# Kernel optimization log

Measured on AMD Instinct MI355X. Metric: run time of the kernel, lower is better.

## Reference

```python
import jax, jax.numpy as jnp
import numpy as np

N = 50000   # nodes
E = 800000  # edges (before self-loops)
IN, H1, H2, OUT = 128, 256, 256, 64


def _gcn_layer(x, src, dst, norm_src, norm_dst, W, b, act):
    # DGL GraphConv, norm='both': D_in^{-1/2} * A^T * (D_out^{-1/2} * x) @ W + b
    x = x * norm_src                                   # [N, d_in]
    m = jax.ops.segment_sum(x[src], dst, num_segments=N)  # gather + scatter-add
    h = (m * norm_dst) @ W + b                         # [N, d_out]
    return act(h) if act is not None else h


def setup_inputs() -> dict:
    key = jax.random.key(0)
    ks = jax.random.split(key, 9)
    feats = jax.random.normal(ks[0], (N, IN), dtype=jnp.float32)
    src = jax.random.randint(ks[1], (E,), 0, N, dtype=jnp.int32)
    dst = jax.random.randint(ks[2], (E,), 0, N, dtype=jnp.int32)
    # avoid pre-existing self-loops (forward removes then re-adds exactly one per node)
    dst = jnp.where(src == dst, (dst + 1) % N, dst)
    def glorot(k, fi, fo):
        lim = float(np.sqrt(6.0 / (fi + fo)))
        return jax.random.uniform(k, (fi, fo), jnp.float32, -lim, lim)
    return {
        "feats": feats,
        "W1": glorot(ks[3], IN, H1), "b1": jnp.zeros((H1,), jnp.float32),
        "W2": glorot(ks[4], H1, H2), "b2": jnp.zeros((H2,), jnp.float32),
        "W3": glorot(ks[5], H2, OUT), "b3": jnp.zeros((OUT,), jnp.float32),
        "src": src, "dst": dst,
    }


def reference(feats, W1, b1, W2, b2, W3, b3, src, dst):
    # add self-loops
    loops = jnp.arange(N, dtype=src.dtype)
    s = jnp.concatenate([src, loops])
    d = jnp.concatenate([dst, loops])
    ones = jnp.ones(s.shape[0], jnp.float32)
    out_deg = jax.ops.segment_sum(ones, s, num_segments=N)
    in_deg = jax.ops.segment_sum(ones, d, num_segments=N)
    norm_src = (out_deg ** -0.5)[:, None]
    norm_dst = (in_deg ** -0.5)[:, None]
    relu = jax.nn.relu
    h = _gcn_layer(feats, s, d, norm_src, norm_dst, W1, b1, relu)
    # dropout p=0.0 (eval) is identity
    h = _gcn_layer(h, s, d, norm_src, norm_dst, W2, b2, relu)
    h = _gcn_layer(h, s, d, norm_src, norm_dst, W3, b3, None)
    return h
```

## Files before the change

### kernel.cpp

```cpp
#include <hip/hip_runtime.h>
#include <hip/hip_fp16.h>
#include <stdint.h>

#define NODES 50000
#define F_IN 128
#define F_H1 256
#define F_H2 256
#define F_OUT 64
#define SLICES 64
#define NPACK (NODES / 2)
#define HPACK (NPACK / 2)

using f32x4    = __attribute__((ext_vector_type(4))) float;
using f16x8    = __attribute__((ext_vector_type(8))) _Float16;
using ushort8v = __attribute__((ext_vector_type(8))) unsigned short;

__global__ __launch_bounds__(512) void k_hist(
    const int* __restrict__ src, const int* __restrict__ dst,
    unsigned* __restrict__ p_out, unsigned* __restrict__ p_in, int e) {
  __shared__ unsigned bins[HPACK];
  const int s = blockIdx.x >> 1;
  const int r = blockIdx.x & 1;
  const int nlo = r * (NODES / 2);
  const int nhi = nlo + NODES / 2;
  const int plo = r * HPACK;
  const int per = (e + SLICES - 1) / SLICES;
  const int beg = s * per;
  const int end = min(e, beg + per);

  for (int j = threadIdx.x; j < HPACK; j += 512) bins[j] = 0;
  __syncthreads();
  for (int i = beg + (int)threadIdx.x; i < end; i += 512) {
    int a = src[i];
    if (a >= nlo && a < nhi)
      atomicAdd(&bins[(a >> 1) - plo], 1u << ((a & 1) << 4));
  }
  __syncthreads();
  for (int j = threadIdx.x; j < HPACK; j += 512)
    p_out[(size_t)s * NPACK + plo + j] = bins[j];
  __syncthreads();

  for (int j = threadIdx.x; j < HPACK; j += 512) bins[j] = 0;
  __syncthreads();
  for (int i = beg + (int)threadIdx.x; i < end; i += 512) {
    int d = dst[i];
    if (d >= nlo && d < nhi)
      atomicAdd(&bins[(d >> 1) - plo], 1u << ((d & 1) << 4));
  }
  __syncthreads();
  for (int j = threadIdx.x; j < HPACK; j += 512)
    p_in[(size_t)s * NPACK + plo + j] = bins[j];
}

__global__ __launch_bounds__(256) void k_degnorm(
    const unsigned* __restrict__ p_out, const unsigned* __restrict__ p_in,
    unsigned* __restrict__ base_in, int* __restrict__ deg_in,
    float* __restrict__ ns, float* __restrict__ nd) {
  int p = blockIdx.x * 256 + threadIdx.x;
  if (p >= NPACK) return;
  unsigned so = 0, si = 0;
#pragma unroll 4
  for (int s = 0; s < SLICES; ++s) {
    so += p_out[(size_t)s * NPACK + p];
    unsigned vi = p_in[(size_t)s * NPACK + p];
    base_in[(size_t)s * NPACK + p] = si;
    si += vi;
  }
  int o0 = (int)(so & 0xFFFFu) + 1, o1 = (int)(so >> 16) + 1;
  int i0 = (int)(si & 0xFFFFu) + 1, i1 = (int)(si >> 16) + 1;
  int n0 = p * 2, n1 = n0 + 1;
  deg_in[n0] = i0; deg_in[n1] = i1;
  ns[n0] = rsqrtf((float)o0); ns[n1] = rsqrtf((float)o1);
  nd[n0] = rsqrtf((float)i0); nd[n1] = rsqrtf((float)i1);
}

__global__ __launch_bounds__(256) void k_scan1(const int* __restrict__ deg_in,
                                               int* __restrict__ psum, int n) {
  int i = blockIdx.x * 256 + threadIdx.x;
  int v = (i < n) ? deg_in[i] - 1 : 0;
#pragma unroll
  for (int o = 1; o < 64; o <<= 1) v += __shfl_xor(v, o);
  __shared__ int ws[4];
  if ((threadIdx.x & 63) == 0) ws[threadIdx.x >> 6] = v;
  __syncthreads();
  if (threadIdx.x == 0) psum[blockIdx.x] = ws[0] + ws[1] + ws[2] + ws[3];
}

__global__ __launch_bounds__(256) void k_scan2(int* __restrict__ psum, int nb) {
  __shared__ int s[256];
  int t = threadIdx.x;
  int v = (t < nb) ? psum[t] : 0;
  s[t] = v;
  __syncthreads();
  for (int o = 1; o < 256; o <<= 1) {
    int u = (t >= o) ? s[t - o] : 0;
    __syncthreads();
    s[t] += u;
    __syncthreads();
  }
  if (t < nb) psum[t] = s[t] - v;
}

__global__ __launch_bounds__(256) void k_scan3(const int* __restrict__ deg_in,
                                               const int* __restrict__ psum,
                                               int* __restrict__ row_ptr, int n) {
  int i = blockIdx.x * 256 + threadIdx.x;
  int lane = threadIdx.x & 63;
  int w = threadIdx.x >> 6;
  int v = (i < n) ? deg_in[i] - 1 : 0;
  int x = v;
#pragma unroll
  for (int o = 1; o < 64; o <<= 1) {
    int u = __shfl_up(x, o);
    if (lane >= o) x += u;
  }
  __shared__ int wsum[4];
  if (lane == 63) wsum[w] = x;
  __syncthreads();
  int woff = 0;
#pragma unroll
  for (int j = 0; j < 4; ++j)
    if (j < w) woff += wsum[j];
  int excl = x - v + woff + psum[blockIdx.x];
  if (i < n) row_ptr[i] = excl;
  if (i == n - 1) row_ptr[n] = excl + v;
}

__global__ __launch_bounds__(512) void k_scatter2(
    const int* __restrict__ src, const int* __restrict__ dst,
    const int* __restrict__ row_ptr, const unsigned* __restrict__ base_in,
    int* __restrict__ csr_src, int e) {
  __shared__ unsigned cur[HPACK];
  const int s = blockIdx.x >> 1;
  const int r = blockIdx.x & 1;
  const int nlo = r * (NODES / 2);
  const int nhi = nlo + NODES / 2;
  const int plo = r * HPACK;
  const int per = (e + SLICES - 1) / SLICES;
  const int beg = s * per;
  const int end = min(e, beg + per);
  for (int j = threadIdx.x; j < HPACK; j += 512)
    cur[j] = base_in[(size_t)s * NPACK + plo + j];
  __syncthreads();
  for (int i = beg + (int)threadIdx.x; i < end; i += 512) {
    int d = dst[i];
    if (d >= nlo && d < nhi) {
      int sh = (d & 1) << 4;
      unsigned old = atomicAdd(&cur[(d >> 1) - plo], 1u << sh);
      int local = (int)((old >> sh) & 0xFFFFu);
      csr_src[row_ptr[d] + local] = src[i];
    }
  }
}

__global__ void k_prescale_h(const float* __restrict__ X, const float* __restrict__ ns,
                             __half* __restrict__ Y, int total4) {
  int i = blockIdx.x * blockDim.x + threadIdx.x;
  if (i < total4) {
    int row = i >> 5;
    float s = ns[row];
    float4 v = reinterpret_cast<const float4*>(X)[i];
    __half2 h0 = __floats2half2_rn(v.x * s, v.y * s);
    __half2 h1 = __floats2half2_rn(v.z * s, v.w * s);
    union { struct { __half2 a, b; } h; uint2 u; } o;
    o.h.a = h0; o.h.b = h1;
    reinterpret_cast<uint2*>(Y)[i] = o.u;
  }
}

__global__ void k_wprep_h(const float* __restrict__ W, __half* __restrict__ Wt,
                          int K, int NOUT) {
  int i = blockIdx.x * blockDim.x + threadIdx.x;
  if (i < K * NOUT) {
    int k = i / NOUT, n = i % NOUT;
    Wt[(size_t)n * K + k] = __float2half_rn(W[i]);
  }
}

template <int HPL> struct raw_t_sel;
template <> struct raw_t_sel<2> { using type = unsigned int; };
template <> struct raw_t_sel<4> { using type = uint2; };
template <> struct raw_t_sel<8> { using type = uint4; };

template <int HPL>
__device__ __forceinline__ typename raw_t_sel<HPL>::type graw(const __half* p) {
  return *reinterpret_cast<const typename raw_t_sel<HPL>::type*>(p);
}
__device__ __forceinline__ void acc_u32(float* acc, unsigned u) {
  union { unsigned u; __half2 h; } a; a.u = u;
  float2 f = __half22float2(a.h);
  acc[0] += f.x; acc[1] += f.y;
}
template <int HPL>
__device__ __forceinline__ void raw_acc(float* acc, typename raw_t_sel<HPL>::type r) {
  if constexpr (HPL == 8) {
    acc_u32(acc + 0, r.x); acc_u32(acc + 2, r.y);
    acc_u32(acc + 4, r.z); acc_u32(acc + 6, r.w);
  } else if constexpr (HPL == 4) {
    acc_u32(acc + 0, r.x); acc_u32(acc + 2, r.y);
  } else {
    acc_u32(acc, r);
  }
}

template <int D, int EPI, bool BIAS, bool OHALF>
__global__ __launch_bounds__(256) void k_spmm_h(
    const __half* __restrict__ X, const int* __restrict__ row_ptr,
    const int* __restrict__ csr_src, const float* __restrict__ nd,
    const float* __restrict__ bias, void* __restrict__ Y, int n) {
  constexpr int LPN = 64 / EPI;
  constexpr int HPL = D / LPN;
  static_assert(HPL >= 2 && HPL <= 8, "bad HPL");
  const int v = (blockIdx.x * blockDim.x + threadIdx.x) >> 6;
  const int lane = threadIdx.x & 63;
  if (v >= n) return;
  const int sub = lane / LPN;
  const int fl = lane % LPN;
  const int off = fl * HPL;
  const __half* __restrict__ Xo = X + off;

  float acc[HPL] = {};
  if (sub == 0) raw_acc<HPL>(acc, graw<HPL>(Xo + (size_t)v * D));

  const int beg = row_ptr[v];
  const int end = row_ptr[v + 1];
#pragma unroll 2
  for (int e = beg; e < end; e += EPI) {
    int ei = e + sub;
    if (ei < end) {
      int u = csr_src[ei];
      raw_acc<HPL>(acc, graw<HPL>(Xo + (size_t)u * D));
    }
  }

#pragma unroll
  for (int o = LPN; o < 64; o <<= 1)
#pragma unroll
    for (int i = 0; i < HPL; ++i) acc[i] += __shfl_xor(acc[i], o);

  if (sub != 0) return;
  const float sc = nd[v];
  float o[HPL];
#pragma unroll
  for (int i = 0; i < HPL; ++i) {
    o[i] = sc * acc[i];
    if (BIAS) o[i] += bias[off + i];
  }

  if constexpr (OHALF) {
    __half* yp = reinterpret_cast<__half*>(Y) + (size_t)v * D + off;
    if constexpr (HPL == 8) {
      union { struct { __half2 a, b, c, d; } h; uint4 u; } pk;
      pk.h.a = __floats2half2_rn(o[0], o[1]);
      pk.h.b = __floats2half2_rn(o[2], o[3]);
      pk.h.c = __floats2half2_rn(o[4], o[5]);
      pk.h.d = __floats2half2_rn(o[6], o[7]);
      *reinterpret_cast<uint4*>(yp) = pk.u;
    } else if constexpr (HPL == 4) {
      union { struct { __half2 a, b; } h; uint2 u; } pk;
      pk.h.a = __floats2half2_rn(o[0], o[1]);
      pk.h.b = __floats2half2_rn(o[2], o[3]);
      *reinterpret_cast<uint2*>(yp) = pk.u;
    } else {
      *reinterpret_cast<__half2*>(yp) = __floats2half2_rn(o[0], o[1]);
    }
  } else {
    float* yp = reinterpret_cast<float*>(Y) + (size_t)v * D + off;
    if constexpr (HPL == 8) {
      *reinterpret_cast<float4*>(yp) = make_float4(o[0], o[1], o[2], o[3]);
      *reinterpret_cast<float4*>(yp + 4) = make_float4(o[4], o[5], o[6], o[7]);
    } else if constexpr (HPL == 4) {
      *reinterpret_cast<float4*>(yp) = make_float4(o[0], o[1], o[2], o[3]);
    } else {
      *reinterpret_cast<float2*>(yp) = make_float2(o[0], o[1]);
    }
  }
}

template <int K, int NOUT, int BM, int WM, int WN, int MF, int NF,
          bool RELU, bool BIAS, bool NSOUT, bool OHALF>
__global__ __launch_bounds__(256) void k_gemm_h(
    const __half* __restrict__ A, const __half* __restrict__ Wt,
    const float* __restrict__ bias, const float* __restrict__ ns,
    void* __restrict__ C, int M) {
  constexpr int BN = WN * NF * 16;
  static_assert(BM == WM * MF * 16, "BM mismatch");
  static_assert(BN == NOUT, "BN must equal NOUT");
  constexpr int LDP = 40;

  __shared__ __half As[BM][LDP];
  __shared__ __half Ws[BN][LDP];

  const int tid = threadIdx.x;
  const int bm = blockIdx.x * BM;
  const int lane = tid & 63;
  const int wave = tid >> 6;
  const int wmi = wave / WN;
  const int wni = wave % WN;
  const int rl = lane & 15;
  const int kg = lane >> 4;
  const int kb = kg * 8;

  f32x4 acc[MF][NF];
#pragma unroll
  for (int m = 0; m < MF; ++m)
#pragma unroll
    for (int n = 0; n < NF; ++n) acc[m][n] = (f32x4){0.f, 0.f, 0.f, 0.f};

  for (int kk = 0; kk < K; kk += 32) {
#pragma unroll
    for (int s0 = 0; s0 < BM * 4; s0 += 256) {
      int s = s0 + tid;
      int r = s >> 2, c8 = (s & 3) << 3;
      int grow = bm + r;
      ushort8v v = (ushort8v){0, 0, 0, 0, 0, 0, 0, 0};
      if (grow < M)
        v = *reinterpret_cast<const ushort8v*>(A + (size_t)grow * K + kk + c8);
      *reinterpret_cast<ushort8v*>(&As[r][c8]) = v;
    }
#pragma unroll
    for (int s0 = 0; s0 < BN * 4; s0 += 256) {
      int s = s0 + tid;
      int nn = s >> 2, k8 = (s & 3) << 3;
      *reinterpret_cast<ushort8v*>(&Ws[nn][k8]) =
          *reinterpret_cast<const ushort8v*>(Wt + (size_t)nn * K + kk + k8);
    }
    __syncthreads();

    f16x8 af[MF], bf[NF];
#pragma unroll
    for (int m = 0; m < MF; ++m) {
      const int r = wmi * MF * 16 + m * 16 + rl;
      af[m] = *reinterpret_cast<const f16x8*>(&As[r][kb]);
    }
#pragma unroll
    for (int n = 0; n < NF; ++n) {
      const int c = wni * NF * 16 + n * 16 + rl;
      bf[n] = *reinterpret_cast<const f16x8*>(&Ws[c][kb]);
    }
#pragma unroll
    for (int m = 0; m < MF; ++m)
#pragma unroll
      for (int n = 0; n < NF; ++n)
        acc[m][n] = __builtin_amdgcn_mfma_f32_16x16x32_f16(af[m], bf[n], acc[m][n], 0, 0, 0);
    __syncthreads();
  }

#pragma unroll
  for (int m = 0; m < MF; ++m) {
#pragma unroll
    for (int n = 0; n < NF; ++n) {
      const int col = wni * NF * 16 + n * 16 + rl;
      const float bb = BIAS ? bias[col] : 0.f;
      const int rowbase = bm + wmi * MF * 16 + m * 16 + kg * 4;
#pragma unroll
      for (int i = 0; i < 4; ++i) {
        int grow = rowbase + i;
        if (grow < M) {
          float val = acc[m][n][i] + bb;
          if (RELU) val = fmaxf(val, 0.f);
          if (NSOUT) val *= ns[grow];
          if constexpr (OHALF)
            reinterpret_cast<__half*>(C)[(size_t)grow * NOUT + col] = __float2half_rn(val);
          else
            reinterpret_cast<float*>(C)[(size_t)grow * NOUT + col] = val;
        }
      }
    }
  }
}

extern "C" void kernel_launch(void* const* d_in, const int* in_sizes, int n_in,
                              void* d_out, int out_size, void* d_ws, size_t ws_size,
                              hipStream_t stream) {
  const float* feats = (const float*)d_in[0];
  const float* W1 = (const float*)d_in[1];
  const float* b1 = (const float*)d_in[2];
  const float* W2 = (const float*)d_in[3];
  const float* b2 = (const float*)d_in[4];
  const float* W3 = (const float*)d_in[5];
  const float* b3 = (const float*)d_in[6];
  const int* src = (const int*)d_in[7];
  const int* dst = (const int*)d_in[8];
  float* out = (float*)d_out;
  const int N = NODES;
  const int E = in_sizes[7];
  const int NB = (N + 255) / 256;

  char* ws = (char*)d_ws;
  size_t off = 0;
  auto alloc = [&](size_t bytes) -> void* {
    void* p = ws + off;
    off += (bytes + 255) & ~(size_t)255;
    return p;
  };
  __half* w0h = (__half*)alloc((size_t)N * 256 * sizeof(__half));
  __half* w1r = (__half*)alloc((size_t)N * 256 * sizeof(__half));
  __half* w2r = (__half*)alloc((size_t)N * 256 * sizeof(__half));
  int* deg_in = (int*)alloc((size_t)N * sizeof(int));
  float* ns = (float*)alloc((size_t)N * sizeof(float));
  float* nd = (float*)alloc((size_t)N * sizeof(float));
  int* row_ptr = (int*)alloc((size_t)(N + 1) * sizeof(int));
  int* csr_src = (int*)alloc((size_t)E * sizeof(int));
  int* psum = (int*)alloc((size_t)NB * sizeof(int));
  unsigned* p_out = (unsigned*)alloc((size_t)SLICES * NPACK * sizeof(unsigned));
  unsigned* p_in = (unsigned*)alloc((size_t)SLICES * NPACK * sizeof(unsigned));
  unsigned* base_in = (unsigned*)alloc((size_t)SLICES * NPACK * sizeof(unsigned));
  __half* wt1 = (__half*)alloc((size_t)F_IN * F_H1 * sizeof(__half));
  __half* wt2 = (__half*)alloc((size_t)F_H1 * F_H2 * sizeof(__half));
  __half* wt3 = (__half*)alloc((size_t)F_H2 * F_OUT * sizeof(__half));
  (void)ws_size; (void)n_in; (void)out_size;

  hipLaunchKernelGGL(k_wprep_h, dim3((F_IN * F_H1 + 255) / 256), dim3(256), 0, stream,
                     W1, wt1, F_IN, F_H1);
  hipLaunchKernelGGL(k_wprep_h, dim3((F_H1 * F_H2 + 255) / 256), dim3(256), 0, stream,
                     W2, wt2, F_H1, F_H2);
  hipLaunchKernelGGL(k_wprep_h, dim3((F_H2 * F_OUT + 255) / 256), dim3(256), 0, stream,
                     W3, wt3, F_H2, F_OUT);

  hipLaunchKernelGGL(k_hist, dim3(SLICES * 2), dim3(512), 0, stream,
                     src, dst, p_out, p_in, E);
  hipLaunchKernelGGL(k_degnorm, dim3((NPACK + 255) / 256), dim3(256), 0, stream,
                     p_out, p_in, base_in, deg_in, ns, nd);
  hipLaunchKernelGGL(k_scan1, dim3(NB), dim3(256), 0, stream, deg_in, psum, N);
  hipLaunchKernelGGL(k_scan2, dim3(1), dim3(256), 0, stream, psum, NB);
  hipLaunchKernelGGL(k_scan3, dim3(NB), dim3(256), 0, stream, deg_in, psum, row_ptr, N);
  hipLaunchKernelGGL(k_scatter2, dim3(SLICES * 2), dim3(512), 0, stream,
                     src, dst, row_ptr, base_in, csr_src, E);

  hipLaunchKernelGGL(k_prescale_h, dim3((N * 32 + 255) / 256), dim3(256), 0, stream,
                     feats, ns, w2r, N * 32);

  auto grid_w = [](int waves) { return dim3((waves + 3) / 4); };

  hipLaunchKernelGGL((k_spmm_h<128, 4, false, true>), grid_w(N), dim3(256), 0, stream,
                     w2r, row_ptr, csr_src, nd, nullptr, w1r, N);
  hipLaunchKernelGGL((k_gemm_h<128, 256, 64, 1, 4, 4, 4, true, true, true, true>),
                     dim3((N + 63) / 64), dim3(256), 0, stream,
                     w1r, wt1, b1, ns, w2r, N);

  hipLaunchKernelGGL((k_spmm_h<256, 2, false, true>), grid_w(N), dim3(256), 0, stream,
                     w2r, row_ptr, csr_src, nd, nullptr, w0h, N);
  hipLaunchKernelGGL((k_gemm_h<256, 256, 64, 1, 4, 4, 4, true, true, true, true>),
                     dim3((N + 63) / 64), dim3(256), 0, stream,
                     w0h, wt2, b2, ns, w1r, N);

  hipLaunchKernelGGL((k_gemm_h<256, 64, 128, 4, 1, 2, 4, false, false, false, true>),
                     dim3((N + 127) / 128), dim3(256), 0, stream,
                     w1r, wt3, nullptr, nullptr, w2r, N);
  hipLaunchKernelGGL((k_spmm_h<64, 4, true, false>), grid_w(N), dim3(256), 0, stream,
                     w2r, row_ptr, csr_src, nd, b3, out, N);
}
```

Baseline: 288.7 us.

## Partition SpMM feature columns across XCDs to keep gather slices L2-resident

Rewrites the SpMM aggregation so that each XCD (selected by blockIdx mod 8) processes one 32-column feature slice for a subset of nodes, using a persistent grid-stride loop. The aim is to shrink each XCD's working set of gathered feature rows so it fits in that XCD's L2, cutting HBM traffic from random neighbour gathers. In exchange, the CSR indices are re-read once per slice, and each lane now loads only 4 bytes per edge, which raises instruction count and lowers memory parallelism per load.

New measurement: 695.9 us. +141.0%, slower.

```diff
diff --git a/kernel.cpp b/kernel.cpp
--- a/kernel.cpp
+++ b/kernel.cpp
@@ -10,6 +10,7 @@
 #define SLICES 64
 #define NPACK (NODES / 2)
 #define HPACK (NPACK / 2)
+#define SPMM_J 128
 
 using f32x4    = __attribute__((ext_vector_type(4))) float;
 using f16x8    = __attribute__((ext_vector_type(8))) _Float16;
@@ -177,102 +178,58 @@
   }
 }
 
-template <int HPL> struct raw_t_sel;
-template <> struct raw_t_sel<2> { using type = unsigned int; };
-template <> struct raw_t_sel<4> { using type = uint2; };
-template <> struct raw_t_sel<8> { using type = uint4; };
-
-template <int HPL>
-__device__ __forceinline__ typename raw_t_sel<HPL>::type graw(const __half* p) {
-  return *reinterpret_cast<const typename raw_t_sel<HPL>::type*>(p);
-}
-__device__ __forceinline__ void acc_u32(float* acc, unsigned u) {
-  union { unsigned u; __half2 h; } a; a.u = u;
-  float2 f = __half22float2(a.h);
-  acc[0] += f.x; acc[1] += f.y;
-}
-template <int HPL>
-__device__ __forceinline__ void raw_acc(float* acc, typename raw_t_sel<HPL>::type r) {
-  if constexpr (HPL == 8) {
-    acc_u32(acc + 0, r.x); acc_u32(acc + 2, r.y);
-    acc_u32(acc + 4, r.z); acc_u32(acc + 6, r.w);
-  } else if constexpr (HPL == 4) {
-    acc_u32(acc + 0, r.x); acc_u32(acc + 2, r.y);
-  } else {
-    acc_u32(acc, r);
-  }
-}
-
-template <int D, int EPI, bool BIAS, bool OHALF>
-__global__ __launch_bounds__(256) void k_spmm_h(
+template <int D, bool BIAS, bool OHALF>
+__global__ __launch_bounds__(256) void k_spmm_x(
     const __half* __restrict__ X, const int* __restrict__ row_ptr,
     const int* __restrict__ csr_src, const float* __restrict__ nd,
     const float* __restrict__ bias, void* __restrict__ Y, int n) {
-  constexpr int LPN = 64 / EPI;
-  constexpr int HPL = D / LPN;
-  static_assert(HPL >= 2 && HPL <= 8, "bad HPL");
-  const int v = (blockIdx.x * blockDim.x + threadIdx.x) >> 6;
-  const int lane = threadIdx.x & 63;
-  if (v >= n) return;
-  const int sub = lane / LPN;
-  const int fl = lane % LPN;
-  const int off = fl * HPL;
+  constexpr int NSL = D / 32;
+  constexpr int G = 8 / NSL;
+  const int xcd = blockIdx.x & 7;
+  const int j = blockIdx.x >> 3;
+  const int s = xcd % NSL;
+  const int g = xcd / NSL;
+  const int npg = (n + G - 1) / G;
+  const int vbeg = g * npg;
+  const int vend = min(n, vbeg + npg);
+  const int wave = (int)(threadIdx.x >> 6);
+  const int lane = (int)(threadIdx.x & 63);
+  const int sub = lane >> 4;
+  const int fl = lane & 15;
+  const int off = s * 32 + fl * 2;
   const __half* __restrict__ Xo = X + off;
-
-  float acc[HPL] = {};
-  if (sub == 0) raw_acc<HPL>(acc, graw<HPL>(Xo + (size_t)v * D));
-
-  const int beg = row_ptr[v];
-  const int end = row_ptr[v + 1];
-#pragma unroll 2
-  for (int e = beg; e < end; e += EPI) {
-    int ei = e + sub;
-    if (ei < end) {
-      int u = csr_src[ei];
-      raw_acc<HPL>(acc, graw<HPL>(Xo + (size_t)u * D));
-    }
-  }
-
-#pragma unroll
-  for (int o = LPN; o < 64; o <<= 1)
-#pragma unroll
-    for (int i = 0; i < HPL; ++i) acc[i] += __shfl_xor(acc[i], o);
-
-  if (sub != 0) return;
-  const float sc = nd[v];
-  float o[HPL];
-#pragma unroll
-  for (int i = 0; i < HPL; ++i) {
-    o[i] = sc * acc[i];
-    if (BIAS) o[i] += bias[off + i];
-  }
-
-  if constexpr (OHALF) {
-    __half* yp = reinterpret_cast<__half*>(Y) + (size_t)v * D + off;
-    if constexpr (HPL == 8) {
-      union { struct { __half2 a, b, c, d; } h; uint4 u; } pk;
-      pk.h.a = __floats2half2_rn(o[0], o[1]);
-      pk.h.b = __floats2half2_rn(o[2], o[3]);
-      pk.h.c = __floats2half2_rn(o[4], o[5]);
-      pk.h.d = __floats2half2_rn(o[6], o[7]);
-      *reinterpret_cast<uint4*>(yp) = pk.u;
-    } else if constexpr (HPL == 4) {
-      union { struct { __half2 a, b; } h; uint2 u; } pk;
-      pk.h.a = __floats2half2_rn(o[0], o[1]);
-      pk.h.b = __floats2half2_rn(o[2], o[3]);
-      *reinterpret_cast<uint2*>(yp) = pk.u;
-    } else {
-      *reinterpret_cast<__half2*>(yp) = __floats2half2_rn(o[0], o[1]);
-    }
-  } else {
-    float* yp = reinterpret_cast<float*>(Y) + (size_t)v * D + off;
-    if constexpr (HPL == 8) {
-      *reinterpret_cast<float4*>(yp) = make_float4(o[0], o[1], o[2], o[3]);
-      *reinterpret_cast<float4*>(yp + 4) = make_float4(o[4], o[5], o[6], o[7]);
-    } else if constexpr (HPL == 4) {
-      *reinterpret_cast<float4*>(yp) = make_float4(o[0], o[1], o[2], o[3]);
-    } else {
-      *reinterpret_cast<float2*>(yp) = make_float2(o[0], o[1]);
+  const int stride = SPMM_J * 4;
+
+  for (int v = vbeg + j * 4 + wave; v < vend; v += stride) {
+    float a0 = 0.f, a1 = 0.f;
+    const int beg = row_ptr[v];
+    const int end_ = row_ptr[v + 1];
+    if (sub == 0) {
+      union { unsigned u; __half2 h; } t;
+      t.u = *reinterpret_cast<const unsigned*>(Xo + (size_t)v * D);
+      float2 f = __half22float2(t.h);
+      a0 = f.x; a1 = f.y;
+    }
+    for (int e = beg + sub; e < end_; e += 4) {
+      int u = csr_src[e];
+      union { unsigned uu; __half2 h; } t;
+      t.uu = *reinterpret_cast<const unsigned*>(Xo + (size_t)u * D);
+      float2 f = __half22float2(t.h);
+      a0 += f.x; a1 += f.y;
+    }
+    a0 += __shfl_xor(a0, 16); a0 += __shfl_xor(a0, 32);
+    a1 += __shfl_xor(a1, 16); a1 += __shfl_xor(a1, 32);
+    if (sub == 0) {
+      const float sc = nd[v];
+      float o0 = sc * a0, o1 = sc * a1;
+      if (BIAS) { o0 += bias[off]; o1 += bias[off + 1]; }
+      if constexpr (OHALF) {
+        *reinterpret_cast<__half2*>(reinterpret_cast<__half*>(Y) + (size_t)v * D + off) =
+            __floats2half2_rn(o0, o1);
+      } else {
+        *reinterpret_cast<float2*>(reinterpret_cast<float*>(Y) + (size_t)v * D + off) =
+            make_float2(o0, o1);
+      }
     }
   }
 }
@@ -431,15 +388,15 @@
   hipLaunchKernelGGL(k_prescale_h, dim3((N * 32 + 255) / 256), dim3(256), 0, stream,
                      feats, ns, w2r, N * 32);
 
-  auto grid_w = [](int waves) { return dim3((waves + 3) / 4); };
-
-  hipLaunchKernelGGL((k_spmm_h<128, 4, false, true>), grid_w(N), dim3(256), 0, stream,
+  const dim3 spmm_grid(8 * SPMM_J);
+
+  hipLaunchKernelGGL((k_spmm_x<128, false, true>), spmm_grid, dim3(256), 0, stream,
                      w2r, row_ptr, csr_src, nd, nullptr, w1r, N);
   hipLaunchKernelGGL((k_gemm_h<128, 256, 64, 1, 4, 4, 4, true, true, true, true>),
                      dim3((N + 63) / 64), dim3(256), 0, stream,
                      w1r, wt1, b1, ns, w2r, N);
 
-  hipLaunchKernelGGL((k_spmm_h<256, 2, false, true>), grid_w(N), dim3(256), 0, stream,
+  hipLaunchKernelGGL((k_spmm_x<256, false, true>), spmm_grid, dim3(256), 0, stream,
                      w2r, row_ptr, csr_src, nd, nullptr, w0h, N);
   hipLaunchKernelGGL((k_gemm_h<256, 256, 64, 1, 4, 4, 4, true, true, true, true>),
                      dim3((N + 63) / 64), dim3(256), 0, stream,
@@ -448,6 +405,6 @@
   hipLaunchKernelGGL((k_gemm_h<256, 64, 128, 4, 1, 2, 4, false, false, false, true>),
                      dim3((N + 127) / 128), dim3(256), 0, stream,
                      w1r, wt3, nullptr, nullptr, w2r, N);
-  hipLaunchKernelGGL((k_spmm_h<64, 4, true, false>), grid_w(N), dim3(256), 0, stream,
+  hipLaunchKernelGGL((k_spmm_x<64, true, false>), spmm_grid, dim3(256), 0, stream,
                      w2r, row_ptr, csr_src, nd, b3, out, N);
 }
```

## Quarter node ranges in CSR build, fuse histograms, and widen SpMM edge parallelism

Applied to the files above, without the earlier changes.

The histogram kernel now splits nodes into four ranges instead of two and fills the out-degree and in-degree bins in one pass over the edges using two shared arrays, doubling the block count. The scatter kernel is switched to the same four-way split. The SpMM kernels process more edges per wave in parallel (EPI doubled), with a 16-half-per-lane load path for the 256-wide layer and a loop with no per-iteration bounds branch. This aims to raise memory-level parallelism in the gathers and cut the CSR build time, at the cost of more registers per lane and more cross-lane shuffle reductions.

Result: faster. 261.8 us (-9.3%).

```diff
diff --git a/kernel.cpp b/kernel.cpp
--- a/kernel.cpp
+++ b/kernel.cpp
@@ -9,47 +9,41 @@
 #define F_OUT 64
 #define SLICES 64
 #define NPACK (NODES / 2)
-#define HPACK (NPACK / 2)
+#define QPACK (NPACK / 4)
 
 using f32x4    = __attribute__((ext_vector_type(4))) float;
 using f16x8    = __attribute__((ext_vector_type(8))) _Float16;
 using ushort8v = __attribute__((ext_vector_type(8))) unsigned short;
 
-__global__ __launch_bounds__(512) void k_hist(
+__global__ __launch_bounds__(512) void k_hist2(
     const int* __restrict__ src, const int* __restrict__ dst,
     unsigned* __restrict__ p_out, unsigned* __restrict__ p_in, int e) {
-  __shared__ unsigned bins[HPACK];
-  const int s = blockIdx.x >> 1;
-  const int r = blockIdx.x & 1;
-  const int nlo = r * (NODES / 2);
-  const int nhi = nlo + NODES / 2;
-  const int plo = r * HPACK;
+  __shared__ unsigned bo[QPACK];
+  __shared__ unsigned bi[QPACK];
+  const int s = blockIdx.x >> 2;
+  const int r = blockIdx.x & 3;
+  const int nlo = r * (NODES / 4);
+  const int nhi = nlo + NODES / 4;
+  const int plo = r * QPACK;
   const int per = (e + SLICES - 1) / SLICES;
   const int beg = s * per;
   const int end = min(e, beg + per);
 
-  for (int j = threadIdx.x; j < HPACK; j += 512) bins[j] = 0;
+  for (int j = threadIdx.x; j < QPACK; j += 512) { bo[j] = 0; bi[j] = 0; }
   __syncthreads();
   for (int i = beg + (int)threadIdx.x; i < end; i += 512) {
     int a = src[i];
     if (a >= nlo && a < nhi)
-      atomicAdd(&bins[(a >> 1) - plo], 1u << ((a & 1) << 4));
-  }
-  __syncthreads();
-  for (int j = threadIdx.x; j < HPACK; j += 512)
-    p_out[(size_t)s * NPACK + plo + j] = bins[j];
-  __syncthreads();
-
-  for (int j = threadIdx.x; j < HPACK; j += 512) bins[j] = 0;
-  __syncthreads();
-  for (int i = beg + (int)threadIdx.x; i < end; i += 512) {
+      atomicAdd(&bo[(a >> 1) - plo], 1u << ((a & 1) << 4));
     int d = dst[i];
     if (d >= nlo && d < nhi)
-      atomicAdd(&bins[(d >> 1) - plo], 1u << ((d & 1) << 4));
-  }
-  __syncthreads();
-  for (int j = threadIdx.x; j < HPACK; j += 512)
-    p_in[(size_t)s * NPACK + plo + j] = bins[j];
+      atomicAdd(&bi[(d >> 1) - plo], 1u << ((d & 1) << 4));
+  }
+  __syncthreads();
+  for (int j = threadIdx.x; j < QPACK; j += 512) {
+    p_out[(size_t)s * NPACK + plo + j] = bo[j];
+    p_in[(size_t)s * NPACK + plo + j] = bi[j];
+  }
 }
 
 __global__ __launch_bounds__(256) void k_degnorm(
@@ -126,20 +120,20 @@
   if (i == n - 1) row_ptr[n] = excl + v;
 }
 
-__global__ __launch_bounds__(512) void k_scatter2(
+__global__ __launch_bounds__(512) void k_scatter4(
     const int* __restrict__ src, const int* __restrict__ dst,
     const int* __restrict__ row_ptr, const unsigned* __restrict__ base_in,
     int* __restrict__ csr_src, int e) {
-  __shared__ unsigned cur[HPACK];
-  const int s = blockIdx.x >> 1;
-  const int r = blockIdx.x & 1;
-  const int nlo = r * (NODES / 2);
-  const int nhi = nlo + NODES / 2;
-  const int plo = r * HPACK;
+  __shared__ unsigned cur[QPACK];
+  const int s = blockIdx.x >> 2;
+  const int r = blockIdx.x & 3;
+  const int nlo = r * (NODES / 4);
+  const int nhi = nlo + NODES / 4;
+  const int plo = r * QPACK;
   const int per = (e + SLICES - 1) / SLICES;
   const int beg = s * per;
   const int end = min(e, beg + per);
-  for (int j = threadIdx.x; j < HPACK; j += 512)
+  for (int j = threadIdx.x; j < QPACK; j += 512)
     cur[j] = base_in[(size_t)s * NPACK + plo + j];
   __syncthreads();
   for (int i = beg + (int)threadIdx.x; i < end; i += 512) {
@@ -177,14 +171,23 @@
   }
 }
 
+struct u32x8s { uint4 a, b; };
 template <int HPL> struct raw_t_sel;
 template <> struct raw_t_sel<2> { using type = unsigned int; };
 template <> struct raw_t_sel<4> { using type = uint2; };
 template <> struct raw_t_sel<8> { using type = uint4; };
+template <> struct raw_t_sel<16> { using type = u32x8s; };
 
 template <int HPL>
 __device__ __forceinline__ typename raw_t_sel<HPL>::type graw(const __half* p) {
-  return *reinterpret_cast<const typename raw_t_sel<HPL>::type*>(p);
+  if constexpr (HPL == 16) {
+    u32x8s r;
+    r.a = *reinterpret_cast<const uint4*>(p);
+    r.b = *reinterpret_cast<const uint4*>(p + 8);
+    return r;
+  } else {
+    return *reinterpret_cast<const typename raw_t_sel<HPL>::type*>(p);
+  }
 }
 __device__ __forceinline__ void acc_u32(float* acc, unsigned u) {
   union { unsigned u; __half2 h; } a; a.u = u;
@@ -193,7 +196,12 @@
 }
 template <int HPL>
 __device__ __forceinline__ void raw_acc(float* acc, typename raw_t_sel<HPL>::type r) {
-  if constexpr (HPL == 8) {
+  if constexpr (HPL == 16) {
+    acc_u32(acc + 0, r.a.x);  acc_u32(acc + 2, r.a.y);
+    acc_u32(acc + 4, r.a.z);  acc_u32(acc + 6, r.a.w);
+    acc_u32(acc + 8, r.b.x);  acc_u32(acc + 10, r.b.y);
+    acc_u32(acc + 12, r.b.z); acc_u32(acc + 14, r.b.w);
+  } else if constexpr (HPL == 8) {
     acc_u32(acc + 0, r.x); acc_u32(acc + 2, r.y);
     acc_u32(acc + 4, r.z); acc_u32(acc + 6, r.w);
   } else if constexpr (HPL == 4) {
@@ -210,7 +218,7 @@
     const float* __restrict__ bias, void* __restrict__ Y, int n) {
   constexpr int LPN = 64 / EPI;
   constexpr int HPL = D / LPN;
-  static_assert(HPL >= 2 && HPL <= 8, "bad HPL");
+  static_assert(HPL >= 2 && HPL <= 16, "bad HPL");
   const int v = (blockIdx.x * blockDim.x + threadIdx.x) >> 6;
   const int lane = threadIdx.x & 63;
   if (v >= n) return;
@@ -225,12 +233,9 @@
   const int beg = row_ptr[v];
   const int end = row_ptr[v + 1];
 #pragma unroll 2
-  for (int e = beg; e < end; e += EPI) {
-    int ei = e + sub;
-    if (ei < end) {
-      int u = csr_src[ei];
-      raw_acc<HPL>(acc, graw<HPL>(Xo + (size_t)u * D));
-    }
+  for (int e = beg + sub; e < end; e += EPI) {
+    int u = csr_src[e];
+    raw_acc<HPL>(acc, graw<HPL>(Xo + (size_t)u * D));
   }
 
 #pragma unroll
@@ -249,7 +254,19 @@
 
   if constexpr (OHALF) {
     __half* yp = reinterpret_cast<__half*>(Y) + (size_t)v * D + off;
-    if constexpr (HPL == 8) {
+    if constexpr (HPL == 16) {
+      union { struct { __half2 a, b, c, d; } h; uint4 u; } p0, p1;
+      p0.h.a = __floats2half2_rn(o[0], o[1]);
+      p0.h.b = __floats2half2_rn(o[2], o[3]);
+      p0.h.c = __floats2half2_rn(o[4], o[5]);
+      p0.h.d = __floats2half2_rn(o[6], o[7]);
+      p1.h.a = __floats2half2_rn(o[8], o[9]);
+      p1.h.b = __floats2half2_rn(o[10], o[11]);
+      p1.h.c = __floats2half2_rn(o[12], o[13]);
+      p1.h.d = __floats2half2_rn(o[14], o[15]);
+      *reinterpret_cast<uint4*>(yp) = p0.u;
+      *reinterpret_cast<uint4*>(yp + 8) = p1.u;
+    } else if constexpr (HPL == 8) {
       union { struct { __half2 a, b, c, d; } h; uint4 u; } pk;
       pk.h.a = __floats2half2_rn(o[0], o[1]);
       pk.h.b = __floats2half2_rn(o[2], o[3]);
@@ -418,14 +435,14 @@
   hipLaunchKernelGGL(k_wprep_h, dim3((F_H2 * F_OUT + 255) / 256), dim3(256), 0, stream,
                      W3, wt3, F_H2, F_OUT);
 
-  hipLaunchKernelGGL(k_hist, dim3(SLICES * 2), dim3(512), 0, stream,
+  hipLaunchKernelGGL(k_hist2, dim3(SLICES * 4), dim3(512), 0, stream,
                      src, dst, p_out, p_in, E);
   hipLaunchKernelGGL(k_degnorm, dim3((NPACK + 255) / 256), dim3(256), 0, stream,
                      p_out, p_in, base_in, deg_in, ns, nd);
   hipLaunchKernelGGL(k_scan1, dim3(NB), dim3(256), 0, stream, deg_in, psum, N);
   hipLaunchKernelGGL(k_scan2, dim3(1), dim3(256), 0, stream, psum, NB);
   hipLaunchKernelGGL(k_scan3, dim3(NB), dim3(256), 0, stream, deg_in, psum, row_ptr, N);
-  hipLaunchKernelGGL(k_scatter2, dim3(SLICES * 2), dim3(512), 0, stream,
+  hipLaunchKernelGGL(k_scatter4, dim3(SLICES * 4), dim3(512), 0, stream,
                      src, dst, row_ptr, base_in, csr_src, E);
 
   hipLaunchKernelGGL(k_prescale_h, dim3((N * 32 + 255) / 256), dim3(256), 0, stream,
@@ -433,13 +450,13 @@
 
   auto grid_w = [](int waves) { return dim3((waves + 3) / 4); };
 
-  hipLaunchKernelGGL((k_spmm_h<128, 4, false, true>), grid_w(N), dim3(256), 0, stream,
+  hipLaunchKernelGGL((k_spmm_h<128, 8, false, true>), grid_w(N), dim3(256), 0, stream,
                      w2r, row_ptr, csr_src, nd, nullptr, w1r, N);
   hipLaunchKernelGGL((k_gemm_h<128, 256, 64, 1, 4, 4, 4, true, true, true, true>),
                      dim3((N + 63) / 64), dim3(256), 0, stream,
                      w1r, wt1, b1, ns, w2r, N);
 
-  hipLaunchKernelGGL((k_spmm_h<256, 2, false, true>), grid_w(N), dim3(256), 0, stream,
+  hipLaunchKernelGGL((k_spmm_h<256, 4, false, true>), grid_w(N), dim3(256), 0, stream,
                      w2r, row_ptr, csr_src, nd, nullptr, w0h, N);
   hipLaunchKernelGGL((k_gemm_h<256, 256, 64, 1, 4, 4, 4, true, true, true, true>),
                      dim3((N + 63) / 64), dim3(256), 0, stream,
@@ -448,6 +465,6 @@
   hipLaunchKernelGGL((k_gemm_h<256, 64, 128, 4, 1, 2, 4, false, false, false, true>),
                      dim3((N + 127) / 128), dim3(256), 0, stream,
                      w1r, wt3, nullptr, nullptr, w2r, N);
-  hipLaunchKernelGGL((k_spmm_h<64, 4, true, false>), grid_w(N), dim3(256), 0, stream,
+  hipLaunchKernelGGL((k_spmm_h<64, 8, true, false>), grid_w(N), dim3(256), 0, stream,
                      w2r, row_ptr, csr_src, nd, b3, out, N);
 }
```
